# Optimization experiments

Hardware: AMD Instinct MI355X
Metric: run time of the kernel (lower is better)

Reference implementation:

```python
import jax, jax.numpy as jnp
import numpy as np


def setup_inputs() -> dict:
    key = jax.random.key(0)
    k1, k2 = jax.random.split(key)
    n, K = 1024, 8
    pred_y = jax.random.normal(k1, (n, K), dtype=jnp.float32)
    true_y = jax.random.randint(k2, (n, K), 0, 2).astype(jnp.int32)  # multi-label 0/1
    return {"pred_y": pred_y, "true_y": true_y}


def reference(pred_y, true_y):
    # mode == 'pairwise2':
    #   sum_{i,j} sum_{a: y[a,i]==1} sum_{b: y[b,j]==0} log(1 + exp(-(pred[a,i] - pred[b,j])))
    #   normalized by |S_pos| * |S_neg| (total counts over the whole label matrix).
    # The double class loop + cartesian_prod is exactly an all-pairs interaction
    # between flattened positive entries and flattened negative entries.
    pos = (true_y == 1)
    neg = (true_y == 0)
    v = pred_y.reshape(-1)                      # [n*K]
    mp = pos.reshape(-1).astype(pred_y.dtype)   # positive-entry mask
    mn = neg.reshape(-1).astype(pred_y.dtype)   # negative-entry mask
    # loss(p - q) = log(1 + exp(-(p - q))) = softplus(q - p)
    diff = v[None, :] - v[:, None]              # [nK, nK]; diff[a, b] = v_b - v_a
    sp = jax.nn.softplus(diff)
    total = jnp.sum(sp * (mp[:, None] * mn[None, :]))
    denom = jnp.sum(mp) * jnp.sum(mn)           # |S_pos| * |S_neg|
    return total / denom
```

## Files before the change

kernel.cpp:

```cpp
#include <hip/hip_runtime.h>

#define GRID 1024
#define PBLK 512
#define RT   16

#define LOG2E 1.4426950408889634f
#define LN2   0.6931471805599453

__device__ __forceinline__ float fast_exp2(float x) {
#if __has_builtin(__builtin_amdgcn_exp2f)
    return __builtin_amdgcn_exp2f(x);
#else
    return exp2f(x);
#endif
}
__device__ __forceinline__ float fast_log2(float x) {
#if __has_builtin(__builtin_amdgcn_logf)
    return __builtin_amdgcn_logf(x);
#else
    return log2f(x);
#endif
}

__global__ __launch_bounds__(PBLK) void pair_kernel(
        const float* __restrict__ v,
        const int* __restrict__ ty,
        float* __restrict__ partials,
        int N) {
    const int tid = threadIdx.x;

    float pa[RT], w[RT];
    const float4* v4  = (const float4*)v;
    const int4*   t4  = (const int4*)ty;
    #pragma unroll
    for (int j = 0; j < RT / 4; ++j) {
        const int q = j * PBLK + tid;
        const float4 vv = v4[q];
        const int4   tt = t4[q];
        pa[4*j+0] = vv.x * LOG2E;  w[4*j+0] = (tt.x == 1) ? 1.0f : 0.0f;
        pa[4*j+1] = vv.y * LOG2E;  w[4*j+1] = (tt.y == 1) ? 1.0f : 0.0f;
        pa[4*j+2] = vv.z * LOG2E;  w[4*j+2] = (tt.z == 1) ? 1.0f : 0.0f;
        pa[4*j+3] = vv.w * LOG2E;  w[4*j+3] = (tt.w == 1) ? 1.0f : 0.0f;
    }

    float acc = 0.0f;
    for (int b = blockIdx.x; b < N; b += GRID) {
        if (ty[b] != 0) continue;
        const float vbl = v[b] * LOG2E;
        #pragma unroll
        for (int r = 0; r < RT; ++r) {
            const float x = vbl - pa[r];
            const float e = fast_exp2(-fabsf(x));
            const float t = fmaxf(x, 0.0f) + fast_log2(1.0f + e);
            acc = fmaf(w[r], t, acc);
        }
    }

    for (int off = 32; off > 0; off >>= 1)
        acc += __shfl_down(acc, off, 64);

    __shared__ float wsum[PBLK / 64];
    const int lane = tid & 63;
    const int wid  = tid >> 6;
    if (lane == 0) wsum[wid] = acc;
    __syncthreads();
    if (tid == 0) {
        float s = 0.0f;
        #pragma unroll
        for (int wdx = 0; wdx < PBLK / 64; ++wdx) s += wsum[wdx];
        partials[blockIdx.x] = s;
    }
}

__global__ __launch_bounds__(PBLK) void finalize_kernel(
        const float* __restrict__ partials, int nparts,
        const int* __restrict__ ty, int N,
        float* __restrict__ out) {
    const int tid = threadIdx.x;

    double s = 0.0;
    for (int k = tid; k < nparts; k += PBLK) s += (double)partials[k];

    int cp = 0, cn = 0;
    for (int k = tid; k < N; k += PBLK) {
        const int t = ty[k];
        cp += (t == 1);
        cn += (t == 0);
    }

    __shared__ double sd[PBLK];
    __shared__ int    sp_[PBLK];
    __shared__ int    sn_[PBLK];
    sd[tid] = s; sp_[tid] = cp; sn_[tid] = cn;
    __syncthreads();
    for (int off = PBLK / 2; off > 0; off >>= 1) {
        if (tid < off) {
            sd[tid]  += sd[tid + off];
            sp_[tid] += sp_[tid + off];
            sn_[tid] += sn_[tid + off];
        }
        __syncthreads();
    }
    if (tid == 0) {
        const double denom = (double)sp_[0] * (double)sn_[0];
        out[0] = (float)(sd[0] * LN2 / denom);
    }
}

extern "C" void kernel_launch(void* const* d_in, const int* in_sizes, int n_in,
                              void* d_out, int out_size, void* d_ws, size_t ws_size,
                              hipStream_t stream) {
    const float* v  = (const float*)d_in[0];
    const int*   ty = (const int*)d_in[1];
    float* out = (float*)d_out;
    const int N = in_sizes[0];

    float* partials = (float*)d_ws;

    pair_kernel<<<GRID, PBLK, 0, stream>>>(v, ty, partials, N);
    finalize_kernel<<<1, PBLK, 0, stream>>>(partials, GRID, ty, N, out);
}
```

Baseline: 72.63 us.

## Replace per-pair log with running product and sentinel masking, batch negative loads

Accumulates the softplus log terms as a product of (1+e) factors per negative element and takes a single log2 per 16 pairs instead of one log per pair. Non-positive row entries are set to a large sentinel so their contribution vanishes without a weight multiply. Loads for several negative columns are batched up front to expose memory-level parallelism. The product of up to 16 factors bounded by 2 stays in float range, with slight rounding differences from summing logs.

```diff
diff --git a/kernel.cpp b/kernel.cpp
--- a/kernel.cpp
+++ b/kernel.cpp
@@ -3,9 +3,11 @@
 #define GRID 1024
 #define PBLK 512
 #define RT   16
+#define BCH  8
 
 #define LOG2E 1.4426950408889634f
 #define LN2   0.6931471805599453
+#define BIGF  1.0e30f
 
 __device__ __forceinline__ float fast_exp2(float x) {
 #if __has_builtin(__builtin_amdgcn_exp2f)
@@ -29,32 +31,50 @@
         int N) {
     const int tid = threadIdx.x;
 
-    float pa[RT], w[RT];
-    const float4* v4  = (const float4*)v;
-    const int4*   t4  = (const int4*)ty;
+    float pa[RT];
+    const float4* v4 = (const float4*)v;
+    const int4*   t4 = (const int4*)ty;
     #pragma unroll
     for (int j = 0; j < RT / 4; ++j) {
         const int q = j * PBLK + tid;
         const float4 vv = v4[q];
         const int4   tt = t4[q];
-        pa[4*j+0] = vv.x * LOG2E;  w[4*j+0] = (tt.x == 1) ? 1.0f : 0.0f;
-        pa[4*j+1] = vv.y * LOG2E;  w[4*j+1] = (tt.y == 1) ? 1.0f : 0.0f;
-        pa[4*j+2] = vv.z * LOG2E;  w[4*j+2] = (tt.z == 1) ? 1.0f : 0.0f;
-        pa[4*j+3] = vv.w * LOG2E;  w[4*j+3] = (tt.w == 1) ? 1.0f : 0.0f;
+        pa[4*j+0] = (tt.x == 1) ? vv.x * LOG2E : BIGF;
+        pa[4*j+1] = (tt.y == 1) ? vv.y * LOG2E : BIGF;
+        pa[4*j+2] = (tt.z == 1) ? vv.z * LOG2E : BIGF;
+        pa[4*j+3] = (tt.w == 1) ? vv.w * LOG2E : BIGF;
     }
 
-    float acc = 0.0f;
-    for (int b = blockIdx.x; b < N; b += GRID) {
-        if (ty[b] != 0) continue;
-        const float vbl = v[b] * LOG2E;
+    float accm = 0.0f;
+    float accl = 0.0f;
+
+    for (int b0 = blockIdx.x; b0 < N; b0 += GRID * BCH) {
+        float vb[BCH];
+        int   tb[BCH];
         #pragma unroll
-        for (int r = 0; r < RT; ++r) {
-            const float x = vbl - pa[r];
-            const float e = fast_exp2(-fabsf(x));
-            const float t = fmaxf(x, 0.0f) + fast_log2(1.0f + e);
-            acc = fmaf(w[r], t, acc);
+        for (int k = 0; k < BCH; ++k) {
+            const int b  = b0 + k * GRID;
+            const bool ok = (b < N);
+            vb[k] = ok ? v[b] * LOG2E : 0.0f;
+            tb[k] = ok ? ty[b] : 1;
+        }
+        #pragma unroll
+        for (int k = 0; k < BCH; ++k) {
+            if (tb[k] != 0) continue;
+            const float vbl = vb[k];
+            float p = 1.0f;
+            #pragma unroll
+            for (int r = 0; r < RT; ++r) {
+                const float x = vbl - pa[r];
+                accm += fmaxf(x, 0.0f);
+                const float e = fast_exp2(-fabsf(x));
+                p = fmaf(p, e, p);
+            }
+            accl += fast_log2(p);
         }
     }
+
+    float acc = accm + accl;
 
     for (int off = 32; off > 0; off >>= 1)
         acc += __shfl_down(acc, off, 64);
```

New measurement: 68.77 us. -5.3%, faster.
